# Optimization experiments

Hardware: AMD Instinct MI355X
Metric: run time of the kernel (lower is better)

## Reference

```python
import jax, jax.numpy as jnp
import numpy as np

BN_EPS = 1e-5
GRID_W = 17  # conv output width hardcoded via lat_idx*17+lon_idx

def _conv(x, w, b, stride):
    y = jax.lax.conv_general_dilated(x, w, (stride, stride), [(1, 1), (1, 1)],
                                     dimension_numbers=("NCHW", "OIHW", "NCHW"))
    return y + b[None, :, None, None]

def _bn_eval(x, g, b):
    # running_mean=0, running_var=1 (fresh BatchNorm in eval mode)
    inv = jnp.float32(1.0 / np.sqrt(1.0 + BN_EPS))
    return x * (g[None, :, None, None] * inv) + b[None, :, None, None]

def setup_inputs() -> dict:
    key = jax.random.key(0)
    ks = iter(jax.random.split(key, 64))
    def rn(shape, s=0.05):
        return jax.random.normal(next(ks), shape, jnp.float32) * s
    B, S, K = 512, 128, 64
    NR = 100000
    inp = {}
    inp["roads"] = jax.random.randint(next(ks), (B, S), 0, NR)
    inp["ratios"] = jax.random.uniform(next(ks), (B, S), jnp.float32) * 0.9 + 0.1
    inp["T"] = jax.random.normal(next(ks), (1, 1, 138, 138), jnp.float32)
    inp["lon_idx"] = jax.random.randint(next(ks), (B, K), 0, 17)
    inp["lat_idx"] = jax.random.randint(next(ks), (B, K), 0, 17)
    inp["lengths"] = jax.random.uniform(next(ks), (NR,), jnp.float32) * 100.0 + 1.0
    inp["map_u"] = jnp.arange(NR, dtype=jnp.int32)
    inp["map_s1"] = jax.random.randint(next(ks), (NR,), 0, 14)
    inp["map_s2"] = jax.random.randint(next(ks), (NR,), 0, 7)
    inp["map_s3"] = jax.random.randint(next(ks), (NR,), 0, 2)
    inp["emb_u"] = rn((NR, 128))
    inp["emb_s1"] = rn((14, 16)); inp["emb_s2"] = rn((7, 8)); inp["emb_s3"] = rn((2, 4))
    inp["rho_w1"] = rn((156, 512)); inp["rho_b1"] = jnp.zeros((512,), jnp.float32)
    inp["rho_w21"] = rn((512, 128)); inp["rho_b21"] = jnp.zeros((128,), jnp.float32)
    inp["conv1_w"] = rn((32, 1, 5, 5)); inp["conv1_b"] = jnp.zeros((32,), jnp.float32)
    inp["bn1_g"] = jnp.ones((32,), jnp.float32); inp["bn1_b"] = jnp.zeros((32,), jnp.float32)
    inp["conv2_w"] = rn((64, 32, 4, 4)); inp["conv2_b"] = jnp.zeros((64,), jnp.float32)
    inp["bn2_g"] = jnp.ones((64,), jnp.float32); inp["bn2_b"] = jnp.zeros((64,), jnp.float32)
    inp["conv3_w"] = rn((128, 64, 4, 4)); inp["conv3_b"] = jnp.zeros((128,), jnp.float32)
    inp["bn3_g"] = jnp.ones((128,), jnp.float32); inp["bn3_b"] = jnp.zeros((128,), jnp.float32)
    inp["f2_w1"] = rn((128, 256)); inp["f2_b1"] = jnp.zeros((256,), jnp.float32)
    inp["f2_w2"] = rn((256, 128)); inp["f2_b2"] = jnp.zeros((128,), jnp.float32)
    inp["f_w1"] = rn((256, 512)); inp["f_b1"] = jnp.zeros((512,), jnp.float32)
    inp["f_w21"] = rn((512, 1)); inp["f_b21"] = jnp.zeros((1,), jnp.float32)
    inp["f_w22"] = rn((512, 1)); inp["f_b22"] = jnp.zeros((1,), jnp.float32)
    return inp

def reference(roads, ratios, T, lon_idx, lat_idx, lengths, map_u, map_s1, map_s2, map_s3,
              emb_u, emb_s1, emb_s2, emb_s3, rho_w1, rho_b1, rho_w21, rho_b21,
              conv1_w, conv1_b, bn1_g, bn1_b, conv2_w, conv2_b, bn2_g, bn2_b,
              conv3_w, conv3_b, bn3_g, bn3_b, f2_w1, f2_b1, f2_w2, f2_b2,
              f_w1, f_b1, f_w21, f_b21, f_w22, f_b22):
    # road lengths / weights
    road_lens = lengths[roads] * ratios               # (B,S)
    l = road_lens.sum(axis=1)                         # (B,)
    w = road_lens / l[:, None]                        # (B,S)
    # ProbRho (eval: dropout=id, reparameterize -> mu)
    u = emb_u[map_u[roads]]                           # (B,S,128)
    s1 = emb_s1[map_s1[roads]]; s2 = emb_s2[map_s2[roads]]; s3 = emb_s3[map_s3[roads]]
    x = jnp.concatenate([u, s1, s2, s3], axis=2)      # (B,S,156)
    h = jax.nn.relu(x @ rho_w1 + rho_b1)
    rho = h @ rho_w21 + rho_b21                       # (B,S,128)
    # ProbTraffic_spatial conv stack
    t = jax.nn.leaky_relu(_bn_eval(_conv(T, conv1_w, conv1_b, 2), bn1_g, bn1_b), 0.1)
    t = jax.nn.leaky_relu(_bn_eval(_conv(t, conv2_w, conv2_b, 2), bn2_g, bn2_b), 0.1)
    t = jax.nn.leaky_relu(_bn_eval(_conv(t, conv3_w, conv3_b, 2), bn3_g, bn3_b), 0.1)  # (1,128,17,17)
    c_flat = jnp.transpose(t[0], (1, 2, 0)).reshape(-1, t.shape[1])  # (289,128)
    # fused segment gather + mean over each trajectory's grid cells
    idx = lat_idx * GRID_W + lon_idx                  # (B,K)
    c_mean = c_flat[idx].mean(axis=1)                 # (B,128)
    h2 = jax.nn.selu(c_mean @ f2_w1 + f2_b1)
    c2 = h2 @ f2_w2 + f2_b2                           # (B,128)
    # ProbTravelTime
    xcat = jnp.concatenate([rho, jnp.broadcast_to(c2[:, None, :], rho.shape)], axis=2)  # (B,S,256)
    h3 = jax.nn.relu(xcat @ f_w1 + f_b1)              # (B,S,512)
    logm = (h3 @ f_w21 + f_b21)[..., 0]               # (B,S)
    logv = (h3 @ f_w22 + f_b22)[..., 0]
    logw = jnp.log(w)
    logm_agg = jax.nn.logsumexp(logm + logw, axis=1)
    logv_agg = jax.nn.logsumexp(logv + 2.0 * logw, axis=1)
    logl = jnp.log(l)
    logmu = logl - logm_agg
    loglam = logl - 3.0 * logm_agg - logv_agg
    return (logmu, loglam)
```

## Files before the change

### kernel.cpp

```cpp
#include <hip/hip_runtime.h>
#include <hip/hip_bf16.h>
#include <math.h>

#define BB 512
#define SS 128
#define NROWS (BB*SS)
#define TMG 128
#define NBLKG (NROWS/TMG)

__device__ __forceinline__ float leaky01(float x){ return x >= 0.f ? x : 0.1f*x; }

#define BN_INV 0.9999950000374997f
#define SELU_A 1.6732632423543772f
#define SELU_S 1.0507009873554805f

typedef __attribute__((ext_vector_type(8))) short short8;
typedef __attribute__((ext_vector_type(4))) float f32x4;

__device__ __forceinline__ unsigned short f2bf(float f) {
    unsigned int u = __float_as_uint(f);
    u += 0x7fff + ((u >> 16) & 1);
    return (unsigned short)(u >> 16);
}
__device__ __forceinline__ unsigned int pk2(float a, float b) {
    __hip_bfloat162 h = __float22bfloat162_rn(make_float2(a, b));
    unsigned int u;
    __builtin_memcpy(&u, &h, 4);
    return u;
}
__device__ __forceinline__ uint2 pack4bf(float a, float b, float c, float d) {
    uint2 r; r.x = pk2(a, b); r.y = pk2(c, d); return r;
}

__device__ __forceinline__ unsigned short* xsp(unsigned short* base, int row, int col) {
    unsigned off = (unsigned)(row*384 + col*2);
    off ^= (unsigned)((row & 7) << 4);
    return (unsigned short*)((char*)base + off);
}
__device__ __forceinline__ unsigned short* h1p(unsigned short* base, int row, int col) {
    unsigned off = (unsigned)(row*1024 + col*2);
    off ^= (unsigned)((row & 7) << 4);
    return (unsigned short*)((char*)base + off);
}
__device__ __forceinline__ unsigned short* xcp(unsigned short* base, int row, int col) {
    unsigned off = (unsigned)(row*256 + col*2);
    off ^= (unsigned)((row & 7) << 4);
    return (unsigned short*)((char*)base + off);
}

#define PREP_N (278528 + 32768 + 131072)
#define PREP_BLOCKS (PREP_N/256)
#define CONV1_BLOCKS 578

__global__ __launch_bounds__(256) void combo1_kernel(
    const float* __restrict__ w1, const float* __restrict__ w21, const float* __restrict__ fw1,
    unsigned short* __restrict__ sw1, unsigned short* __restrict__ sw21, unsigned short* __restrict__ sw3,
    const float* __restrict__ c2w_in, const float* __restrict__ c3w_in,
    float* __restrict__ w2t, float* __restrict__ w3t,
    const float* __restrict__ T, const float* __restrict__ cw,
    const float* __restrict__ cbias, const float* __restrict__ g,
    const float* __restrict__ bb, float* __restrict__ out)
{
    if (blockIdx.x < PREP_BLOCKS) {
        int t = blockIdx.x*256 + threadIdx.x;
        if (t < 81920) {
            int j = t & 7; int r = t >> 3; int lane = r & 63; r >>= 6;
            int ks = r % 5; int nt = r / 5;
            int n = nt*16 + (lane & 15);
            int k = ks*32 + (lane >> 4)*8 + j;
            float v = (k < 156) ? w1[k*512 + n] : 0.f;
            sw1[t] = f2bf(v);
        } else if (t < 147456) {
            int u = t - 81920;
            int j = u & 7; int r = u >> 3; int lane = r & 63; r >>= 6;
            int ks = r & 15; int nt = r >> 4;
            int d = nt*16 + (lane & 15);
            int k = ks*32 + (lane >> 4)*8 + j;
            sw21[u] = f2bf(w21[k*128 + d]);
        } else if (t < 278528) {
            int u = t - 147456;
            int j = u & 7; int r = u >> 3; int lane = r & 63; r >>= 6;
            int ks = r & 7; int nt = r >> 3;
            int n = nt*16 + (lane & 15);
            int k = ks*32 + (lane >> 4)*8 + j;
            sw3[u] = f2bf(fw1[k*512 + n]);
        } else if (t < 278528 + 32768) {
            int u = t - 278528;
            int oc = u >> 9; int r = u & 511;
            int kk = r >> 5; int ic = r & 31;
            w2t[u] = c2w_in[oc*512 + ic*16 + kk];
        } else {
            int u = t - (278528 + 32768);
            int oc = u >> 10; int r = u & 1023;
            int kk = r >> 6; int ic = r & 63;
            w3t[u] = c3w_in[oc*1024 + ic*16 + kk];
        }
    } else {
        int t = (blockIdx.x - PREP_BLOCKS)*256 + threadIdx.x;
        if (t >= 32*68*68) return;
        int oc  = t & 31;
        int pos = t >> 5;
        int oy = pos / 68, ox = pos % 68;
        float acc = cbias[oc];
        #pragma unroll
        for (int ky=0; ky<5; ++ky) {
            int iy = oy*2 - 1 + ky;
            if (iy < 0 || iy >= 138) continue;
            #pragma unroll
            for (int kx=0; kx<5; ++kx) {
                int ix = ox*2 - 1 + kx;
                if (ix < 0 || ix >= 138) continue;
                acc += cw[oc*25 + ky*5 + kx] * T[iy*138 + ix];
            }
        }
        acc = acc * (g[oc]*BN_INV) + bb[oc];
        out[pos*32 + oc] = leaky01(acc);
    }
}

__global__ __launch_bounds__(256) void conv2_kernel(
    const float* __restrict__ in,
    const float* __restrict__ w2t,
    const float* __restrict__ bias, const float* __restrict__ g,
    const float* __restrict__ bb, float* __restrict__ out)
{
    int gid = blockIdx.x*256 + threadIdx.x;
    if (gid >= 64*34*34*4) return;
    int icg = gid & 3;
    int o   = gid >> 2;
    int oc  = o & 63;
    int pos = o >> 6;
    int oy = pos / 34, ox = pos % 34;
    float acc = 0.f;
    #pragma unroll
    for (int ky=0; ky<4; ++ky) {
        int iy = oy*2 - 1 + ky;
        if (iy < 0 || iy >= 68) continue;
        #pragma unroll
        for (int kx=0; kx<4; ++kx) {
            int ix = ox*2 - 1 + kx;
            if (ix < 0 || ix >= 68) continue;
            const float* ip = &in[(iy*68+ix)*32 + icg*8];
            const float* wp = &w2t[oc*512 + (ky*4+kx)*32 + icg*8];
            float4 i0 = *(const float4*)ip, i1 = *(const float4*)(ip+4);
            float4 w0 = *(const float4*)wp, w1v = *(const float4*)(wp+4);
            acc += i0.x*w0.x + i0.y*w0.y + i0.z*w0.z + i0.w*w0.w
                 + i1.x*w1v.x + i1.y*w1v.y + i1.z*w1v.z + i1.w*w1v.w;
        }
    }
    acc += __shfl_xor(acc, 1, 64);
    acc += __shfl_xor(acc, 2, 64);
    if (icg == 0) {
        acc = (acc + bias[oc]) * (g[oc]*BN_INV) + bb[oc];
        out[pos*64 + oc] = leaky01(acc);
    }
}

__global__ __launch_bounds__(256) void conv3_kernel(
    const float* __restrict__ in,
    const float* __restrict__ w3t,
    const float* __restrict__ bias, const float* __restrict__ g,
    const float* __restrict__ bb, float* __restrict__ outT)
{
    int gid = blockIdx.x*256 + threadIdx.x;
    if (gid >= 128*289*8) return;
    int icg = gid & 7;
    int o   = gid >> 3;
    int oc  = o & 127;
    int pos = o >> 7;
    int oy = pos / 17, ox = pos % 17;
    float acc = 0.f;
    #pragma unroll
    for (int ky=0; ky<4; ++ky) {
        int iy = oy*2 - 1 + ky;
        if (iy < 0 || iy >= 34) continue;
        #pragma unroll
        for (int kx=0; kx<4; ++kx) {
            int ix = ox*2 - 1 + kx;
            if (ix < 0 || ix >= 34) continue;
            const float* ip = &in[(iy*34+ix)*64 + icg*8];
            const float* wp = &w3t[oc*1024 + (ky*4+kx)*64 + icg*8];
            float4 i0 = *(const float4*)ip, i1 = *(const float4*)(ip+4);
            float4 w0 = *(const float4*)wp, w1v = *(const float4*)(wp+4);
            acc += i0.x*w0.x + i0.y*w0.y + i0.z*w0.z + i0.w*w0.w
                 + i1.x*w1v.x + i1.y*w1v.y + i1.z*w1v.z + i1.w*w1v.w;
        }
    }
    acc += __shfl_xor(acc, 1, 64);
    acc += __shfl_xor(acc, 2, 64);
    acc += __shfl_xor(acc, 4, 64);
    if (icg == 0) {
        acc = (acc + bias[oc]) * (g[oc]*BN_INV) + bb[oc];
        outT[pos*128 + oc] = leaky01(acc);
    }
}

__global__ __launch_bounds__(256) void cmh2c2_kernel(
    const float* __restrict__ t3T, const int* __restrict__ lat, const int* __restrict__ lon,
    const float* __restrict__ w1, const float* __restrict__ b1,
    const float* __restrict__ w2, const float* __restrict__ b2,
    const float* __restrict__ fw1, const float* __restrict__ fb1,
    float* __restrict__ cvb)
{
    __shared__ int   ps[64];
    __shared__ float part[256];
    __shared__ float cms[128];
    __shared__ float h2s[256];
    __shared__ float c2s[128];
    const int b = blockIdx.x;
    const int tid = threadIdx.x;
    if (tid < 64) ps[tid] = lat[b*64+tid]*17 + lon[b*64+tid];
    __syncthreads();
    {
        int d = tid & 127, half = tid >> 7;
        float s = 0.f;
        #pragma unroll 8
        for (int k=0; k<32; ++k) s += t3T[ps[half*32+k]*128 + d];
        part[tid] = s;
    }
    __syncthreads();
    if (tid < 128) cms[tid] = (part[tid] + part[tid+128]) * (1.f/64.f);
    __syncthreads();
    {
        float acc = b1[tid];
        #pragma unroll 8
        for (int k=0; k<128; ++k) acc += cms[k] * w1[k*256 + tid];
        h2s[tid] = acc > 0.f ? SELU_S*acc : SELU_S*SELU_A*(expf(acc)-1.f);
    }
    __syncthreads();
    {
        int d = tid & 127, half = tid >> 7;
        float acc = 0.f;
        #pragma unroll 8
        for (int k=0; k<128; ++k) acc += h2s[half*128 + k] * w2[(half*128+k)*128 + d];
        part[tid] = acc;
    }
    __syncthreads();
    if (tid < 128) c2s[tid] = part[tid] + part[tid+128] + b2[tid];
    __syncthreads();
    {
        float a0 = fb1[tid], a1 = fb1[tid + 256];
        #pragma unroll 8
        for (int k=0; k<128; ++k) {
            float c = c2s[k];
            a0 += c * fw1[(128+k)*512 + tid];
            a1 += c * fw1[(128+k)*512 + 256 + tid];
        }
        cvb[b*512 + tid]       = a0;
        cvb[b*512 + 256 + tid] = a1;
    }
}

__global__ __launch_bounds__(1024, 4) void mega_kernel(
    const int* __restrict__ roads, const float* __restrict__ ratios,
    const float* __restrict__ lengths,
    const int* __restrict__ map_u, const int* __restrict__ map_s1,
    const int* __restrict__ map_s2, const int* __restrict__ map_s3,
    const float* __restrict__ emb_u, const float* __restrict__ emb_s1,
    const float* __restrict__ emb_s2, const float* __restrict__ emb_s3,
    const unsigned short* __restrict__ sw1, const float* __restrict__ b1,
    const unsigned short* __restrict__ sw21, const float* __restrict__ b21,
    const unsigned short* __restrict__ sw3, const float* __restrict__ cvb,
    const float* __restrict__ fw21, const float* __restrict__ fb21,
    const float* __restrict__ fw22, const float* __restrict__ fb22,
    float* __restrict__ out)
{
    __shared__ unsigned short buf[65536];
    float* pmv = (float*)buf;
    float* fin = (float*)buf + 4096;

    const int tid  = threadIdx.x;
    const int wid  = tid >> 6;
    const int lane = tid & 63;
    const int lo   = lane & 15;
    const int hi   = lane >> 4;
    const int b    = blockIdx.x;
    const int r0   = b * TMG;
    const int nt2  = wid >> 1;
    const int rh   = wid & 1;

    short8 afp00 = *(const short8*)&sw1[((wid*2+0)*5 + 0)*512 + lane*8];
    short8 afp10 = *(const short8*)&sw1[((wid*2+1)*5 + 0)*512 + lane*8];
    short8 afp01 = *(const short8*)&sw1[((wid*2+0)*5 + 1)*512 + lane*8];
    short8 afp11 = *(const short8*)&sw1[((wid*2+1)*5 + 1)*512 + lane*8];

    {
        int row = tid >> 3, seg = tid & 7;
        int road = roads[r0 + row];
        const float* src = emb_u + (long)map_u[road]*128 + seg*16;
        #pragma unroll
        for (int i=0;i<4;++i) {
            float4 v = *(const float4*)&src[i*4];
            *(uint2*)xsp(buf, row, seg*16 + i*4) = pack4bf(v.x, v.y, v.z, v.w);
        }
    }
    for (int idx = tid; idx < 128*32; idx += 1024) {
        int row = idx >> 5, k2 = idx & 31;
        int road = roads[r0 + row];
        float v;
        if      (k2 < 16) v = emb_s1[map_s1[road]*16 + k2];
        else if (k2 < 24) v = emb_s2[map_s2[road]*8  + (k2-16)];
        else if (k2 < 28) v = emb_s3[map_s3[road]*4  + (k2-24)];
        else              v = 0.f;
        *xsp(buf, row, 128 + k2) = f2bf(v);
    }
    __syncthreads();

    f32x4 acc1[2][8];
    {
        #pragma unroll
        for (int mt=0;mt<2;++mt)
            #pragma unroll
            for (int rg=0;rg<8;++rg) acc1[mt][rg]=(f32x4)(0.f);
        short8 a0c = afp00, a1c = afp10, a0n = afp01, a1n = afp11;
        #pragma unroll
        for (int ks=0; ks<5; ++ks) {
            short8 a0f = a0c, a1f = a1c;
            if (ks < 3) {
                a0f = *(const short8*)&sw1[((wid*2+0)*5 + ks+2)*512 + lane*8];
                a1f = *(const short8*)&sw1[((wid*2+1)*5 + ks+2)*512 + lane*8];
            }
            const int kb = ks*32 + hi*8;
            short8 bf[4];
            #pragma unroll
            for (int rg=0;rg<4;++rg) bf[rg] = *(const short8*)xsp(buf, rg*16+lo, kb);
            #pragma unroll
            for (int rg=0;rg<4;++rg) {
                acc1[0][rg] = __builtin_amdgcn_mfma_f32_16x16x32_bf16(a0c, bf[rg], acc1[0][rg], 0,0,0);
                acc1[1][rg] = __builtin_amdgcn_mfma_f32_16x16x32_bf16(a1c, bf[rg], acc1[1][rg], 0,0,0);
            }
            #pragma unroll
            for (int rg=0;rg<4;++rg) bf[rg] = *(const short8*)xsp(buf, (4+rg)*16+lo, kb);
            #pragma unroll
            for (int rg=0;rg<4;++rg) {
                acc1[0][4+rg] = __builtin_amdgcn_mfma_f32_16x16x32_bf16(a0c, bf[rg], acc1[0][4+rg], 0,0,0);
                acc1[1][4+rg] = __builtin_amdgcn_mfma_f32_16x16x32_bf16(a1c, bf[rg], acc1[1][4+rg], 0,0,0);
            }
            a0c = a0n; a1c = a1n; a0n = a0f; a1n = a1f;
        }
    }
    __syncthreads();

    short8 a2q0, a2q1, a2q2, a2q3;
    {
        a2q0 = *(const short8*)&sw21[(nt2*16 + 0)*512 + lane*8];
        a2q1 = *(const short8*)&sw21[(nt2*16 + 1)*512 + lane*8];
        a2q2 = *(const short8*)&sw21[(nt2*16 + 2)*512 + lane*8];
        a2q3 = *(const short8*)&sw21[(nt2*16 + 3)*512 + lane*8];
        const int n0 = wid * 32;
        #pragma unroll
        for (int mt=0;mt<2;++mt) {
            const int nb = n0 + mt*16 + hi*4;
            float4 bias = *(const float4*)&b1[nb];
            const float* bp = (const float*)&bias;
            #pragma unroll
            for (int rg=0;rg<8;++rg) {
                const float* a = (const float*)&acc1[mt][rg];
                float y0 = fmaxf(a[0]+bp[0], 0.f), y1 = fmaxf(a[1]+bp[1], 0.f);
                float y2 = fmaxf(a[2]+bp[2], 0.f), y3 = fmaxf(a[3]+bp[3], 0.f);
                *(uint2*)h1p(buf, rg*16+lo, nb) = pack4bf(y0,y1,y2,y3);
            }
        }
    }
    __syncthreads();

    f32x4 acc2[4];
    {
        #pragma unroll
        for (int i=0;i<4;++i) acc2[i]=(f32x4)(0.f);
        #pragma unroll
        for (int ks=0; ks<16; ++ks) {
            short8 a_use = a2q0;
            a2q0 = a2q1; a2q1 = a2q2; a2q2 = a2q3;
            if (ks < 12)
                a2q3 = *(const short8*)&sw21[(nt2*16 + ks+4)*512 + lane*8];
            const int kb = ks*32 + hi*8;
            short8 bf[4];
            #pragma unroll
            for (int i=0;i<4;++i) bf[i] = *(const short8*)h1p(buf, (rh*4+i)*16+lo, kb);
            #pragma unroll
            for (int i=0;i<4;++i)
                acc2[i] = __builtin_amdgcn_mfma_f32_16x16x32_bf16(a_use, bf[i], acc2[i], 0,0,0);
        }
    }
    __syncthreads();

    short8 a3c0, a3c1, a3n0, a3n1;
    {
        a3c0 = *(const short8*)&sw3[((wid*2+0)*8 + 0)*512 + lane*8];
        a3c1 = *(const short8*)&sw3[((wid*2+1)*8 + 0)*512 + lane*8];
        a3n0 = *(const short8*)&sw3[((wid*2+0)*8 + 1)*512 + lane*8];
        a3n1 = *(const short8*)&sw3[((wid*2+1)*8 + 1)*512 + lane*8];
        const int nb = nt2*16 + hi*4;
        float4 bias = *(const float4*)&b21[nb];
        const float* bp = (const float*)&bias;
        #pragma unroll
        for (int i=0;i<4;++i) {
            const float* a = (const float*)&acc2[i];
            *(uint2*)xcp(buf, (rh*4+i)*16+lo, nb) =
                pack4bf(a[0]+bp[0], a[1]+bp[1], a[2]+bp[2], a[3]+bp[3]);
        }
    }
    __syncthreads();

    float sm[8], sv[8];
    {
        const int n0 = wid * 32;
        f32x4 acc[2][8];
        #pragma unroll
        for (int mt=0;mt<2;++mt)
            #pragma unroll
            for (int rg=0;rg<8;++rg) acc[mt][rg]=(f32x4)(0.f);
        #pragma unroll
        for (int ks=0; ks<4; ++ks) {
            short8 c0f = a3c0, c1f = a3c1;
            if (ks < 2) {
                c0f = *(const short8*)&sw3[((wid*2+0)*8 + ks+2)*512 + lane*8];
                c1f = *(const short8*)&sw3[((wid*2+1)*8 + ks+2)*512 + lane*8];
            }
            const int kb = ks*32 + hi*8;
            short8 bf[4];
            #pragma unroll
            for (int rg=0;rg<4;++rg) bf[rg] = *(const short8*)xcp(buf, rg*16+lo, kb);
            #pragma unroll
            for (int rg=0;rg<4;++rg) {
                acc[0][rg] = __builtin_amdgcn_mfma_f32_16x16x32_bf16(a3c0, bf[rg], acc[0][rg], 0,0,0);
                acc[1][rg] = __builtin_amdgcn_mfma_f32_16x16x32_bf16(a3c1, bf[rg], acc[1][rg], 0,0,0);
            }
            #pragma unroll
            for (int rg=0;rg<4;++rg) bf[rg] = *(const short8*)xcp(buf, (4+rg)*16+lo, kb);
            #pragma unroll
            for (int rg=0;rg<4;++rg) {
                acc[0][4+rg] = __builtin_amdgcn_mfma_f32_16x16x32_bf16(a3c0, bf[rg], acc[0][4+rg], 0,0,0);
                acc[1][4+rg] = __builtin_amdgcn_mfma_f32_16x16x32_bf16(a3c1, bf[rg], acc[1][4+rg], 0,0,0);
            }
            a3c0 = a3n0; a3c1 = a3n1; a3n0 = c0f; a3n1 = c1f;
        }
        #pragma unroll
        for (int rg=0;rg<8;++rg){ sm[rg]=0.f; sv[rg]=0.f; }
        #pragma unroll
        for (int mt=0;mt<2;++mt) {
            const int nb = n0 + mt*16 + hi*4;
            float4 bias = *(const float4*)&cvb[b*512 + nb];
            float4 wm   = *(const float4*)&fw21[nb];
            float4 wv   = *(const float4*)&fw22[nb];
            const float *bp=(const float*)&bias, *wmp=(const float*)&wm, *wvp=(const float*)&wv;
            #pragma unroll
            for (int rg=0;rg<8;++rg) {
                const float* a = (const float*)&acc[mt][rg];
                #pragma unroll
                for (int j=0;j<4;++j) {
                    float y = fmaxf(a[j]+bp[j], 0.f);
                    sm[rg] += y*wmp[j];
                    sv[rg] += y*wvp[j];
                }
            }
        }
        #pragma unroll
        for (int rg=0;rg<8;++rg) {
            sm[rg] += __shfl_xor(sm[rg], 16, 64); sm[rg] += __shfl_xor(sm[rg], 32, 64);
            sv[rg] += __shfl_xor(sv[rg], 16, 64); sv[rg] += __shfl_xor(sv[rg], 32, 64);
        }
    }
    __syncthreads();
    if (hi == 0) {
        #pragma unroll
        for (int rg=0;rg<8;++rg) {
            pmv[wid*128 + rg*16 + lo]        = sm[rg];
            pmv[2048 + wid*128 + rg*16 + lo] = sv[rg];
        }
    }
    __syncthreads();

    float rl = 0.f, am = 0.f, av = 0.f;
    if (tid < 128) {
        float s_m = 0.f, s_v = 0.f;
        #pragma unroll
        for (int w=0; w<16; ++w) {
            s_m += pmv[w*128 + tid];
            s_v += pmv[2048 + w*128 + tid];
        }
        s_m += fb21[0]; s_v += fb22[0];
        int gi = r0 + tid;
        rl = lengths[roads[gi]] * ratios[gi];
        float ws = rl;
        #pragma unroll
        for (int off=32; off; off>>=1) ws += __shfl_xor(ws, off, 64);
        if (lane == 0) fin[wid] = ws;
        am = s_m; av = s_v;
    }
    __syncthreads();
    if (tid < 128) {
        float l = fin[0] + fin[1];
        float logl = logf(l);
        float lw = logf(rl) - logl;
        am += lw; av += 2.f*lw;
        float mm = am, mv = av;
        #pragma unroll
        for (int off=32; off; off>>=1) { mm = fmaxf(mm, __shfl_xor(mm, off, 64)); mv = fmaxf(mv, __shfl_xor(mv, off, 64)); }
        if (lane == 0) { fin[2+wid] = mm; fin[4+wid] = mv; fin[8+wid] = logl; }
    }
    __syncthreads();
    if (tid < 128) {
        float mm = fmaxf(fin[2], fin[3]);
        float mv = fmaxf(fin[4], fin[5]);
        float se = expf(am - mm), sev = expf(av - mv);
        #pragma unroll
        for (int off=32; off; off>>=1) { se += __shfl_xor(se, off, 64); sev += __shfl_xor(sev, off, 64); }
        if (lane == 0) { fin[10+wid] = se; fin[12+wid] = sev; }
    }
    __syncthreads();
    if (tid == 0) {
        float mm = fmaxf(fin[2], fin[3]);
        float mv = fmaxf(fin[4], fin[5]);
        float lsem = logf(fin[10] + fin[11]) + mm;
        float lsev = logf(fin[12] + fin[13]) + mv;
        float logl = fin[8];
        out[b]       = logl - lsem;
        out[512 + b] = logl - 3.f*lsem - lsev;
    }
}

extern "C" void kernel_launch(void* const* d_in, const int* in_sizes, int n_in,
                              void* d_out, int out_size, void* d_ws, size_t ws_size,
                              hipStream_t stream) {
    const int*   roads   = (const int*)  d_in[0];
    const float* ratios  = (const float*)d_in[1];
    const float* T       = (const float*)d_in[2];
    const int*   lon_idx = (const int*)  d_in[3];
    const int*   lat_idx = (const int*)  d_in[4];
    const float* lengths = (const float*)d_in[5];
    const int*   map_u   = (const int*)  d_in[6];
    const int*   map_s1  = (const int*)  d_in[7];
    const int*   map_s2  = (const int*)  d_in[8];
    const int*   map_s3  = (const int*)  d_in[9];
    const float* emb_u   = (const float*)d_in[10];
    const float* emb_s1  = (const float*)d_in[11];
    const float* emb_s2  = (const float*)d_in[12];
    const float* emb_s3  = (const float*)d_in[13];
    const float* rho_w1  = (const float*)d_in[14];
    const float* rho_b1  = (const float*)d_in[15];
    const float* rho_w21 = (const float*)d_in[16];
    const float* rho_b21 = (const float*)d_in[17];
    const float* conv1_w = (const float*)d_in[18];
    const float* conv1_b = (const float*)d_in[19];
    const float* bn1_g   = (const float*)d_in[20];
    const float* bn1_b   = (const float*)d_in[21];
    const float* conv2_w = (const float*)d_in[22];
    const float* conv2_b = (const float*)d_in[23];
    const float* bn2_g   = (const float*)d_in[24];
    const float* bn2_b   = (const float*)d_in[25];
    const float* conv3_w = (const float*)d_in[26];
    const float* conv3_b = (const float*)d_in[27];
    const float* bn3_g   = (const float*)d_in[28];
    const float* bn3_b   = (const float*)d_in[29];
    const float* f2_w1   = (const float*)d_in[30];
    const float* f2_b1   = (const float*)d_in[31];
    const float* f2_w2   = (const float*)d_in[32];
    const float* f2_b2   = (const float*)d_in[33];
    const float* f_w1    = (const float*)d_in[34];
    const float* f_b1    = (const float*)d_in[35];
    const float* f_w21   = (const float*)d_in[36];
    const float* f_b21   = (const float*)d_in[37];
    const float* f_w22   = (const float*)d_in[38];
    const float* f_b22   = (const float*)d_in[39];

    float* ws    = (float*)d_ws;
    float* t1    = ws;
    float* t2    = t1 + 147968;
    float* t3T   = t2 + 73984;
    float* cvb   = t3T + 36992;
    float* w2t   = cvb + 262144;
    float* w3t   = w2t + 32768;
    unsigned short* sw1  = (unsigned short*)(w3t + 131072);
    unsigned short* sw21 = sw1 + 81920;
    unsigned short* sw3  = sw21 + 65536;

    combo1_kernel<<<PREP_BLOCKS + CONV1_BLOCKS, 256, 0, stream>>>(
        rho_w1, rho_w21, f_w1, sw1, sw21, sw3,
        conv2_w, conv3_w, w2t, w3t,
        T, conv1_w, conv1_b, bn1_g, bn1_b, t1);
    conv2_kernel<<<(64*34*34*4 + 255)/256, 256, 0, stream>>>(t1, w2t, conv2_b, bn2_g, bn2_b, t2);
    conv3_kernel<<<(128*289*8 + 255)/256, 256, 0, stream>>>(t2, w3t, conv3_b, bn3_g, bn3_b, t3T);
    cmh2c2_kernel<<<512, 256, 0, stream>>>(t3T, lat_idx, lon_idx, f2_w1, f2_b1, f2_w2, f2_b2,
                                           f_w1, f_b1, cvb);
    mega_kernel<<<NBLKG, 1024, 0, stream>>>(roads, ratios, lengths,
                                            map_u, map_s1, map_s2, map_s3,
                                            emb_u, emb_s1, emb_s2, emb_s3,
                                            sw1, rho_b1, sw21, rho_b21,
                                            sw3, cvb, f_w21, f_b21, f_w22, f_b22,
                                            (float*)d_out);
}
```

Baseline: 117.1 us.

## Fuse context MLP into mega kernel, halve row tile, combine halves via atomics

Removes the separate cmh2c2 kernel and has each mega_kernel block recompute the grid-cell mean, the SELU MLP and the context bias into shared memory. The row tile drops from 128 to 64 rows per block with 512 threads, so two blocks share one trajectory. Their partial log-sum-exp terms are rewritten as plain sums of rl*exp(logit) and merged through a global buffer and an atomic counter, which is zeroed in the first kernel. This saves a launch and the cvb round trip through memory, but every block now repeats the small MLP (twice per trajectory). The exp without max-subtraction also risks overflow.

```diff
diff --git a/kernel.cpp b/kernel.cpp
--- a/kernel.cpp
+++ b/kernel.cpp
@@ -5,7 +5,7 @@
 #define BB 512
 #define SS 128
 #define NROWS (BB*SS)
-#define TMG 128
+#define TMG 64
 #define NBLKG (NROWS/TMG)
 
 __device__ __forceinline__ float leaky01(float x){ return x >= 0.f ? x : 0.1f*x; }
@@ -59,7 +59,8 @@
     float* __restrict__ w2t, float* __restrict__ w3t,
     const float* __restrict__ T, const float* __restrict__ cw,
     const float* __restrict__ cbias, const float* __restrict__ g,
-    const float* __restrict__ bb, float* __restrict__ out)
+    const float* __restrict__ bb, float* __restrict__ out,
+    int* __restrict__ cnt)
 {
     if (blockIdx.x < PREP_BLOCKS) {
         int t = blockIdx.x*256 + threadIdx.x;
@@ -95,6 +96,8 @@
             int kk = r >> 6; int ic = r & 63;
             w3t[u] = c3w_in[oc*1024 + ic*16 + kk];
         }
+    } else if (blockIdx.x == PREP_BLOCKS + CONV1_BLOCKS) {
+        if (threadIdx.x < 256) { cnt[threadIdx.x] = 0; cnt[256 + threadIdx.x] = 0; }
     } else {
         int t = (blockIdx.x - PREP_BLOCKS)*256 + threadIdx.x;
         if (t >= 32*68*68) return;
@@ -195,63 +198,7 @@
     }
 }
 
-__global__ __launch_bounds__(256) void cmh2c2_kernel(
-    const float* __restrict__ t3T, const int* __restrict__ lat, const int* __restrict__ lon,
-    const float* __restrict__ w1, const float* __restrict__ b1,
-    const float* __restrict__ w2, const float* __restrict__ b2,
-    const float* __restrict__ fw1, const float* __restrict__ fb1,
-    float* __restrict__ cvb)
-{
-    __shared__ int   ps[64];
-    __shared__ float part[256];
-    __shared__ float cms[128];
-    __shared__ float h2s[256];
-    __shared__ float c2s[128];
-    const int b = blockIdx.x;
-    const int tid = threadIdx.x;
-    if (tid < 64) ps[tid] = lat[b*64+tid]*17 + lon[b*64+tid];
-    __syncthreads();
-    {
-        int d = tid & 127, half = tid >> 7;
-        float s = 0.f;
-        #pragma unroll 8
-        for (int k=0; k<32; ++k) s += t3T[ps[half*32+k]*128 + d];
-        part[tid] = s;
-    }
-    __syncthreads();
-    if (tid < 128) cms[tid] = (part[tid] + part[tid+128]) * (1.f/64.f);
-    __syncthreads();
-    {
-        float acc = b1[tid];
-        #pragma unroll 8
-        for (int k=0; k<128; ++k) acc += cms[k] * w1[k*256 + tid];
-        h2s[tid] = acc > 0.f ? SELU_S*acc : SELU_S*SELU_A*(expf(acc)-1.f);
-    }
-    __syncthreads();
-    {
-        int d = tid & 127, half = tid >> 7;
-        float acc = 0.f;
-        #pragma unroll 8
-        for (int k=0; k<128; ++k) acc += h2s[half*128 + k] * w2[(half*128+k)*128 + d];
-        part[tid] = acc;
-    }
-    __syncthreads();
-    if (tid < 128) c2s[tid] = part[tid] + part[tid+128] + b2[tid];
-    __syncthreads();
-    {
-        float a0 = fb1[tid], a1 = fb1[tid + 256];
-        #pragma unroll 8
-        for (int k=0; k<128; ++k) {
-            float c = c2s[k];
-            a0 += c * fw1[(128+k)*512 + tid];
-            a1 += c * fw1[(128+k)*512 + 256 + tid];
-        }
-        cvb[b*512 + tid]       = a0;
-        cvb[b*512 + 256 + tid] = a1;
-    }
-}
-
-__global__ __launch_bounds__(1024, 4) void mega_kernel(
+__global__ __launch_bounds__(512, 4) void mega_kernel(
     const int* __restrict__ roads, const float* __restrict__ ratios,
     const float* __restrict__ lengths,
     const int* __restrict__ map_u, const int* __restrict__ map_s1,
@@ -260,30 +207,39 @@
     const float* __restrict__ emb_s2, const float* __restrict__ emb_s3,
     const unsigned short* __restrict__ sw1, const float* __restrict__ b1,
     const unsigned short* __restrict__ sw21, const float* __restrict__ b21,
-    const unsigned short* __restrict__ sw3, const float* __restrict__ cvb,
+    const unsigned short* __restrict__ sw3,
+    const float* __restrict__ t3T, const int* __restrict__ lat, const int* __restrict__ lon,
+    const float* __restrict__ f2w1, const float* __restrict__ f2b1,
+    const float* __restrict__ f2w2, const float* __restrict__ f2b2,
+    const float* __restrict__ fw1raw, const float* __restrict__ fb1,
     const float* __restrict__ fw21, const float* __restrict__ fb21,
     const float* __restrict__ fw22, const float* __restrict__ fb22,
-    float* __restrict__ out)
+    float* __restrict__ Pbuf, int* __restrict__ cnt, float* __restrict__ out)
 {
-    __shared__ unsigned short buf[65536];
-    float* pmv = (float*)buf;
-    float* fin = (float*)buf + 4096;
+    __shared__ __align__(16) unsigned char smem[69888];
+    unsigned short* buf = (unsigned short*)smem;
+    float* cvs = (float*)(smem + 65536);
+    int*   ps  = (int*)(smem + 67584);
+    float* cms = (float*)(smem + 67840);
+    float* h2s = (float*)(smem + 68352);
+    float* c2s = (float*)(smem + 69376);
+    float* pmv = (float*)smem;
 
     const int tid  = threadIdx.x;
     const int wid  = tid >> 6;
     const int lane = tid & 63;
     const int lo   = lane & 15;
     const int hi   = lane >> 4;
-    const int b    = blockIdx.x;
-    const int r0   = b * TMG;
-    const int nt2  = wid >> 1;
-    const int rh   = wid & 1;
-
-    short8 afp00 = *(const short8*)&sw1[((wid*2+0)*5 + 0)*512 + lane*8];
-    short8 afp10 = *(const short8*)&sw1[((wid*2+1)*5 + 0)*512 + lane*8];
-    short8 afp01 = *(const short8*)&sw1[((wid*2+0)*5 + 1)*512 + lane*8];
-    short8 afp11 = *(const short8*)&sw1[((wid*2+1)*5 + 1)*512 + lane*8];
-
+    const int blk  = blockIdx.x;
+    const int b    = blk >> 1;
+    const int r0   = blk * TMG;
+
+    short8 afc[4];
+    #pragma unroll
+    for (int mt=0;mt<4;++mt)
+        afc[mt] = *(const short8*)&sw1[((wid*4+mt)*5 + 0)*512 + lane*8];
+
+    if (tid < 64) ps[tid] = lat[b*64+tid]*17 + lon[b*64+tid];
     {
         int row = tid >> 3, seg = tid & 7;
         int road = roads[r0 + row];
@@ -294,7 +250,9 @@
             *(uint2*)xsp(buf, row, seg*16 + i*4) = pack4bf(v.x, v.y, v.z, v.w);
         }
     }
-    for (int idx = tid; idx < 128*32; idx += 1024) {
+    #pragma unroll
+    for (int it=0; it<4; ++it) {
+        int idx = tid + it*512;
         int row = idx >> 5, k2 = idx & 31;
         int road = roads[r0 + row];
         float v;
@@ -306,59 +264,81 @@
     }
     __syncthreads();
 
-    f32x4 acc1[2][8];
-    {
-        #pragma unroll
-        for (int mt=0;mt<2;++mt)
-            #pragma unroll
-            for (int rg=0;rg<8;++rg) acc1[mt][rg]=(f32x4)(0.f);
-        short8 a0c = afp00, a1c = afp10, a0n = afp01, a1n = afp11;
+    if (tid < 128) {
+        float s = 0.f;
+        #pragma unroll 8
+        for (int k=0; k<64; ++k) s += t3T[ps[k]*128 + tid];
+        cms[tid] = s * (1.f/64.f);
+    }
+    __syncthreads();
+    if (tid < 256) {
+        float a = f2b1[tid];
+        #pragma unroll 8
+        for (int k=0; k<128; ++k) a += cms[k] * f2w1[k*256 + tid];
+        h2s[tid] = a > 0.f ? SELU_S*a : SELU_S*SELU_A*(expf(a)-1.f);
+    }
+    __syncthreads();
+    if (tid < 128) {
+        float a = f2b2[tid];
+        #pragma unroll 8
+        for (int k=0; k<256; ++k) a += h2s[k] * f2w2[k*128 + tid];
+        c2s[tid] = a;
+    }
+    __syncthreads();
+    {
+        float a = fb1[tid];
+        #pragma unroll 8
+        for (int k=0; k<128; ++k) a += c2s[k] * fw1raw[(128+k)*512 + tid];
+        cvs[tid] = a;
+    }
+
+    f32x4 acc1[4][4];
+    {
+        #pragma unroll
+        for (int mt=0;mt<4;++mt)
+            #pragma unroll
+            for (int rt=0;rt<4;++rt) acc1[mt][rt]=(f32x4)(0.f);
         #pragma unroll
         for (int ks=0; ks<5; ++ks) {
-            short8 a0f = a0c, a1f = a1c;
-            if (ks < 3) {
-                a0f = *(const short8*)&sw1[((wid*2+0)*5 + ks+2)*512 + lane*8];
-                a1f = *(const short8*)&sw1[((wid*2+1)*5 + ks+2)*512 + lane*8];
+            short8 afn[4];
+            if (ks < 4) {
+                #pragma unroll
+                for (int mt=0;mt<4;++mt)
+                    afn[mt] = *(const short8*)&sw1[((wid*4+mt)*5 + ks+1)*512 + lane*8];
             }
             const int kb = ks*32 + hi*8;
             short8 bf[4];
             #pragma unroll
-            for (int rg=0;rg<4;++rg) bf[rg] = *(const short8*)xsp(buf, rg*16+lo, kb);
-            #pragma unroll
-            for (int rg=0;rg<4;++rg) {
-                acc1[0][rg] = __builtin_amdgcn_mfma_f32_16x16x32_bf16(a0c, bf[rg], acc1[0][rg], 0,0,0);
-                acc1[1][rg] = __builtin_amdgcn_mfma_f32_16x16x32_bf16(a1c, bf[rg], acc1[1][rg], 0,0,0);
-            }
-            #pragma unroll
-            for (int rg=0;rg<4;++rg) bf[rg] = *(const short8*)xsp(buf, (4+rg)*16+lo, kb);
-            #pragma unroll
-            for (int rg=0;rg<4;++rg) {
-                acc1[0][4+rg] = __builtin_amdgcn_mfma_f32_16x16x32_bf16(a0c, bf[rg], acc1[0][4+rg], 0,0,0);
-                acc1[1][4+rg] = __builtin_amdgcn_mfma_f32_16x16x32_bf16(a1c, bf[rg], acc1[1][4+rg], 0,0,0);
-            }
-            a0c = a0n; a1c = a1n; a0n = a0f; a1n = a1f;
-        }
-    }
-    __syncthreads();
-
-    short8 a2q0, a2q1, a2q2, a2q3;
-    {
-        a2q0 = *(const short8*)&sw21[(nt2*16 + 0)*512 + lane*8];
-        a2q1 = *(const short8*)&sw21[(nt2*16 + 1)*512 + lane*8];
-        a2q2 = *(const short8*)&sw21[(nt2*16 + 2)*512 + lane*8];
-        a2q3 = *(const short8*)&sw21[(nt2*16 + 3)*512 + lane*8];
-        const int n0 = wid * 32;
-        #pragma unroll
-        for (int mt=0;mt<2;++mt) {
+            for (int rt=0;rt<4;++rt) bf[rt] = *(const short8*)xsp(buf, rt*16+lo, kb);
+            #pragma unroll
+            for (int mt=0;mt<4;++mt)
+                #pragma unroll
+                for (int rt=0;rt<4;++rt)
+                    acc1[mt][rt] = __builtin_amdgcn_mfma_f32_16x16x32_bf16(afc[mt], bf[rt], acc1[mt][rt], 0,0,0);
+            if (ks < 4) {
+                #pragma unroll
+                for (int mt=0;mt<4;++mt) afc[mt] = afn[mt];
+            }
+        }
+    }
+    __syncthreads();
+
+    short8 a2c, a2n;
+    {
+        a2c = *(const short8*)&sw21[(wid*16 + 0)*512 + lane*8];
+        a2n = *(const short8*)&sw21[(wid*16 + 1)*512 + lane*8];
+        const int n0 = wid * 64;
+        #pragma unroll
+        for (int mt=0;mt<4;++mt) {
             const int nb = n0 + mt*16 + hi*4;
             float4 bias = *(const float4*)&b1[nb];
             const float* bp = (const float*)&bias;
             #pragma unroll
-            for (int rg=0;rg<8;++rg) {
-                const float* a = (const float*)&acc1[mt][rg];
+            for (int rt=0;rt<4;++rt) {
+                const float* a = (const float*)&acc1[mt][rt];
                 float y0 = fmaxf(a[0]+bp[0], 0.f), y1 = fmaxf(a[1]+bp[1], 0.f);
                 float y2 = fmaxf(a[2]+bp[2], 0.f), y3 = fmaxf(a[3]+bp[3], 0.f);
-                *(uint2*)h1p(buf, rg*16+lo, nb) = pack4bf(y0,y1,y2,y3);
+                *(uint2*)h1p(buf, rt*16+lo, nb) = pack4bf(y0,y1,y2,y3);
             }
         }
     }
@@ -368,16 +348,16 @@
     {
         #pragma unroll
         for (int i=0;i<4;++i) acc2[i]=(f32x4)(0.f);
-        #pragma unroll
+        #pragma unroll 4
         for (int ks=0; ks<16; ++ks) {
-            short8 a_use = a2q0;
-            a2q0 = a2q1; a2q1 = a2q2; a2q2 = a2q3;
-            if (ks < 12)
-                a2q3 = *(const short8*)&sw21[(nt2*16 + ks+4)*512 + lane*8];
+            short8 a_use = a2c;
+            a2c = a2n;
+            if (ks < 14)
+                a2n = *(const short8*)&sw21[(wid*16 + ks+2)*512 + lane*8];
             const int kb = ks*32 + hi*8;
             short8 bf[4];
             #pragma unroll
-            for (int i=0;i<4;++i) bf[i] = *(const short8*)h1p(buf, (rh*4+i)*16+lo, kb);
+            for (int i=0;i<4;++i) bf[i] = *(const short8*)h1p(buf, i*16+lo, kb);
             #pragma unroll
             for (int i=0;i<4;++i)
                 acc2[i] = __builtin_amdgcn_mfma_f32_16x16x32_bf16(a_use, bf[i], acc2[i], 0,0,0);
@@ -385,139 +365,127 @@
     }
     __syncthreads();
 
-    short8 a3c0, a3c1, a3n0, a3n1;
-    {
-        a3c0 = *(const short8*)&sw3[((wid*2+0)*8 + 0)*512 + lane*8];
-        a3c1 = *(const short8*)&sw3[((wid*2+1)*8 + 0)*512 + lane*8];
-        a3n0 = *(const short8*)&sw3[((wid*2+0)*8 + 1)*512 + lane*8];
-        a3n1 = *(const short8*)&sw3[((wid*2+1)*8 + 1)*512 + lane*8];
-        const int nb = nt2*16 + hi*4;
+    short8 a3c[4];
+    {
+        #pragma unroll
+        for (int mt=0;mt<4;++mt)
+            a3c[mt] = *(const short8*)&sw3[((wid*4+mt)*8 + 0)*512 + lane*8];
+        const int nb = wid*16 + hi*4;
         float4 bias = *(const float4*)&b21[nb];
         const float* bp = (const float*)&bias;
         #pragma unroll
         for (int i=0;i<4;++i) {
             const float* a = (const float*)&acc2[i];
-            *(uint2*)xcp(buf, (rh*4+i)*16+lo, nb) =
+            *(uint2*)xcp(buf, i*16+lo, nb) =
                 pack4bf(a[0]+bp[0], a[1]+bp[1], a[2]+bp[2], a[3]+bp[3]);
         }
     }
     __syncthreads();
 
-    float sm[8], sv[8];
-    {
-        const int n0 = wid * 32;
-        f32x4 acc[2][8];
-        #pragma unroll
-        for (int mt=0;mt<2;++mt)
-            #pragma unroll
-            for (int rg=0;rg<8;++rg) acc[mt][rg]=(f32x4)(0.f);
+    float sm[4], sv[4];
+    {
+        f32x4 acc[4][4];
+        #pragma unroll
+        for (int mt=0;mt<4;++mt)
+            #pragma unroll
+            for (int rt=0;rt<4;++rt) acc[mt][rt]=(f32x4)(0.f);
         #pragma unroll
         for (int ks=0; ks<4; ++ks) {
-            short8 c0f = a3c0, c1f = a3c1;
-            if (ks < 2) {
-                c0f = *(const short8*)&sw3[((wid*2+0)*8 + ks+2)*512 + lane*8];
-                c1f = *(const short8*)&sw3[((wid*2+1)*8 + ks+2)*512 + lane*8];
+            short8 a3n[4];
+            if (ks < 3) {
+                #pragma unroll
+                for (int mt=0;mt<4;++mt)
+                    a3n[mt] = *(const short8*)&sw3[((wid*4+mt)*8 + ks+1)*512 + lane*8];
             }
             const int kb = ks*32 + hi*8;
             short8 bf[4];
             #pragma unroll
-            for (int rg=0;rg<4;++rg) bf[rg] = *(const short8*)xcp(buf, rg*16+lo, kb);
-            #pragma unroll
-            for (int rg=0;rg<4;++rg) {
-                acc[0][rg] = __builtin_amdgcn_mfma_f32_16x16x32_bf16(a3c0, bf[rg], acc[0][rg], 0,0,0);
-                acc[1][rg] = __builtin_amdgcn_mfma_f32_16x16x32_bf16(a3c1, bf[rg], acc[1][rg], 0,0,0);
-            }
-            #pragma unroll
-            for (int rg=0;rg<4;++rg) bf[rg] = *(const short8*)xcp(buf, (4+rg)*16+lo, kb);
-            #pragma unroll
-            for (int rg=0;rg<4;++rg) {
-                acc[0][4+rg] = __builtin_amdgcn_mfma_f32_16x16x32_bf16(a3c0, bf[rg], acc[0][4+rg], 0,0,0);
-                acc[1][4+rg] = __builtin_amdgcn_mfma_f32_16x16x32_bf16(a3c1, bf[rg], acc[1][4+rg], 0,0,0);
-            }
-            a3c0 = a3n0; a3c1 = a3n1; a3n0 = c0f; a3n1 = c1f;
-        }
-        #pragma unroll
-        for (int rg=0;rg<8;++rg){ sm[rg]=0.f; sv[rg]=0.f; }
-        #pragma unroll
-        for (int mt=0;mt<2;++mt) {
-            const int nb = n0 + mt*16 + hi*4;
-            float4 bias = *(const float4*)&cvb[b*512 + nb];
+            for (int rt=0;rt<4;++rt) bf[rt] = *(const short8*)xcp(buf, rt*16+lo, kb);
+            #pragma unroll
+            for (int mt=0;mt<4;++mt)
+                #pragma unroll
+                for (int rt=0;rt<4;++rt)
+                    acc[mt][rt] = __builtin_amdgcn_mfma_f32_16x16x32_bf16(a3c[mt], bf[rt], acc[mt][rt], 0,0,0);
+            if (ks < 3) {
+                #pragma unroll
+                for (int mt=0;mt<4;++mt) a3c[mt] = a3n[mt];
+            }
+        }
+        #pragma unroll
+        for (int rt=0;rt<4;++rt){ sm[rt]=0.f; sv[rt]=0.f; }
+        #pragma unroll
+        for (int mt=0;mt<4;++mt) {
+            const int nb = wid*64 + mt*16 + hi*4;
+            float4 bias = *(const float4*)&cvs[nb];
             float4 wm   = *(const float4*)&fw21[nb];
             float4 wv   = *(const float4*)&fw22[nb];
             const float *bp=(const float*)&bias, *wmp=(const float*)&wm, *wvp=(const float*)&wv;
             #pragma unroll
-            for (int rg=0;rg<8;++rg) {
-                const float* a = (const float*)&acc[mt][rg];
+            for (int rt=0;rt<4;++rt) {
+                const float* a = (const float*)&acc[mt][rt];
                 #pragma unroll
                 for (int j=0;j<4;++j) {
                     float y = fmaxf(a[j]+bp[j], 0.f);
-                    sm[rg] += y*wmp[j];
-                    sv[rg] += y*wvp[j];
+                    sm[rt] += y*wmp[j];
+                    sv[rt] += y*wvp[j];
                 }
             }
         }
         #pragma unroll
-        for (int rg=0;rg<8;++rg) {
-            sm[rg] += __shfl_xor(sm[rg], 16, 64); sm[rg] += __shfl_xor(sm[rg], 32, 64);
-            sv[rg] += __shfl_xor(sv[rg], 16, 64); sv[rg] += __shfl_xor(sv[rg], 32, 64);
+        for (int rt=0;rt<4;++rt) {
+            sm[rt] += __shfl_xor(sm[rt], 16, 64); sm[rt] += __shfl_xor(sm[rt], 32, 64);
+            sv[rt] += __shfl_xor(sv[rt], 16, 64); sv[rt] += __shfl_xor(sv[rt], 32, 64);
         }
     }
     __syncthreads();
     if (hi == 0) {
         #pragma unroll
-        for (int rg=0;rg<8;++rg) {
-            pmv[wid*128 + rg*16 + lo]        = sm[rg];
-            pmv[2048 + wid*128 + rg*16 + lo] = sv[rg];
-        }
-    }
-    __syncthreads();
-
-    float rl = 0.f, am = 0.f, av = 0.f;
-    if (tid < 128) {
+        for (int rt=0;rt<4;++rt) {
+            pmv[wid*64 + rt*16 + lo]       = sm[rt];
+            pmv[512 + wid*64 + rt*16 + lo] = sv[rt];
+        }
+    }
+    __syncthreads();
+
+    if (tid < 64) {
         float s_m = 0.f, s_v = 0.f;
         #pragma unroll
-        for (int w=0; w<16; ++w) {
-            s_m += pmv[w*128 + tid];
-            s_v += pmv[2048 + w*128 + tid];
+        for (int w=0; w<8; ++w) {
+            s_m += pmv[w*64 + tid];
+            s_v += pmv[512 + w*64 + tid];
         }
         s_m += fb21[0]; s_v += fb22[0];
         int gi = r0 + tid;
-        rl = lengths[roads[gi]] * ratios[gi];
-        float ws = rl;
-        #pragma unroll
-        for (int off=32; off; off>>=1) ws += __shfl_xor(ws, off, 64);
-        if (lane == 0) fin[wid] = ws;
-        am = s_m; av = s_v;
-    }
-    __syncthreads();
-    if (tid < 128) {
-        float l = fin[0] + fin[1];
-        float logl = logf(l);
-        float lw = logf(rl) - logl;
-        am += lw; av += 2.f*lw;
-        float mm = am, mv = av;
-        #pragma unroll
-        for (int off=32; off; off>>=1) { mm = fmaxf(mm, __shfl_xor(mm, off, 64)); mv = fmaxf(mv, __shfl_xor(mv, off, 64)); }
-        if (lane == 0) { fin[2+wid] = mm; fin[4+wid] = mv; fin[8+wid] = logl; }
-    }
-    __syncthreads();
-    if (tid < 128) {
-        float mm = fmaxf(fin[2], fin[3]);
-        float mv = fmaxf(fin[4], fin[5]);
-        float se = expf(am - mm), sev = expf(av - mv);
-        #pragma unroll
-        for (int off=32; off; off>>=1) { se += __shfl_xor(se, off, 64); sev += __shfl_xor(sev, off, 64); }
-        if (lane == 0) { fin[10+wid] = se; fin[12+wid] = sev; }
-    }
-    __syncthreads();
-    if (tid == 0) {
-        float mm = fmaxf(fin[2], fin[3]);
-        float mv = fmaxf(fin[4], fin[5]);
-        float lsem = logf(fin[10] + fin[11]) + mm;
-        float lsev = logf(fin[12] + fin[13]) + mv;
-        float logl = fin[8];
-        out[b]       = logl - lsem;
-        out[512 + b] = logl - 3.f*lsem - lsev;
+        float rl = lengths[roads[gi]] * ratios[gi];
+        float pl = rl;
+        float p1 = rl * expf(s_m);
+        float p2 = rl * rl * expf(s_v);
+        #pragma unroll
+        for (int off=32; off; off>>=1) {
+            pl += __shfl_xor(pl, off, 64);
+            p1 += __shfl_xor(p1, off, 64);
+            p2 += __shfl_xor(p2, off, 64);
+        }
+        if (tid == 0) {
+            atomicExch(&Pbuf[blk*3+0], pl);
+            atomicExch(&Pbuf[blk*3+1], p1);
+            atomicExch(&Pbuf[blk*3+2], p2);
+            __threadfence();
+            int old = atomicAdd(&cnt[b], 1);
+            if (old == 1) {
+                __threadfence();
+                int pb = (blk^1)*3;
+                float plo = atomicAdd(&Pbuf[pb+0], 0.f);
+                float p1o = atomicAdd(&Pbuf[pb+1], 0.f);
+                float p2o = atomicAdd(&Pbuf[pb+2], 0.f);
+                float L  = pl + plo;
+                float S1 = p1 + p1o;
+                float S2 = p2 + p2o;
+                float logl = logf(L), ls1 = logf(S1), ls2 = logf(S2);
+                out[b]       = 2.f*logl - ls1;
+                out[512 + b] = 6.f*logl - 3.f*ls1 - ls2;
+            }
+        }
     }
 }
 
@@ -569,25 +537,26 @@
     float* t1    = ws;
     float* t2    = t1 + 147968;
     float* t3T   = t2 + 73984;
-    float* cvb   = t3T + 36992;
-    float* w2t   = cvb + 262144;
+    float* w2t   = t3T + 36992;
     float* w3t   = w2t + 32768;
-    unsigned short* sw1  = (unsigned short*)(w3t + 131072);
+    float* Pbuf  = w3t + 131072;
+    int*   cnt   = (int*)(Pbuf + 3072);
+    unsigned short* sw1  = (unsigned short*)(cnt + 512);
     unsigned short* sw21 = sw1 + 81920;
     unsigned short* sw3  = sw21 + 65536;
 
-    combo1_kernel<<<PREP_BLOCKS + CONV1_BLOCKS, 256, 0, stream>>>(
+    combo1_kernel<<<PREP_BLOCKS + CONV1_BLOCKS + 1, 256, 0, stream>>>(
         rho_w1, rho_w21, f_w1, sw1, sw21, sw3,
         conv2_w, conv3_w, w2t, w3t,
-        T, conv1_w, conv1_b, bn1_g, bn1_b, t1);
+        T, conv1_w, conv1_b, bn1_g, bn1_b, t1, cnt);
     conv2_kernel<<<(64*34*34*4 + 255)/256, 256, 0, stream>>>(t1, w2t, conv2_b, bn2_g, bn2_b, t2);
     conv3_kernel<<<(128*289*8 + 255)/256, 256, 0, stream>>>(t2, w3t, conv3_b, bn3_g, bn3_b, t3T);
-    cmh2c2_kernel<<<512, 256, 0, stream>>>(t3T, lat_idx, lon_idx, f2_w1, f2_b1, f2_w2, f2_b2,
-                                           f_w1, f_b1, cvb);
-    mega_kernel<<<NBLKG, 1024, 0, stream>>>(roads, ratios, lengths,
-                                            map_u, map_s1, map_s2, map_s3,
-                                            emb_u, emb_s1, emb_s2, emb_s3,
-                                            sw1, rho_b1, sw21, rho_b21,
-                                            sw3, cvb, f_w21, f_b21, f_w22, f_b22,
-                                            (float*)d_out);
-}
+    mega_kernel<<<NBLKG, 512, 0, stream>>>(roads, ratios, lengths,
+                                           map_u, map_s1, map_s2, map_s3,
+                                           emb_u, emb_s1, emb_s2, emb_s3,
+                                           sw1, rho_b1, sw21, rho_b21, sw3,
+                                           t3T, lat_idx, lon_idx,
+                                           f2_w1, f2_b1, f2_w2, f2_b2,
+                                           f_w1, f_b1, f_w21, f_b21, f_w22, f_b22,
+                                           Pbuf, cnt, (float*)d_out);
+}
```

New measurement: 201.6 us. +72.1%, slower.
